# Performance work log

Hardware: AMD Instinct MI355X
Metric: run time of the kernel (lower is better)

Reference implementation:

```python
import jax, jax.numpy as jnp
import numpy as np

N, T, ENC_H, ATT_H, DEC_H, OUT, SPK = 32, 4096, 512, 256, 512, 80, 64
ATT_RANGE = 10
KW = 31  # conv kernel width, padding 15


def softsign(x):
    return x / (1.0 + jnp.abs(x))


def setup_inputs() -> dict:
    key = jax.random.key(0)
    ks = jax.random.split(key, 20)
    lengths_enc = jax.random.randint(ks[0], (N,), 2048, T + 1)
    pos = jnp.arange(T)
    prev_attention = jax.random.uniform(ks[1], (N, T, 1), jnp.float32)
    # zero attention beyond valid length (so argmax lies within length, as in practice)
    prev_attention = prev_attention * (pos[None, :, None] < lengths_enc[:, None, None])
    s = 0.05
    inp = {
        "input_enc": jax.random.normal(ks[2], (N, T, ENC_H), jnp.float32),
        "input_dec": jax.random.normal(ks[3], (N, 1, OUT), jnp.float32),
        "prev_attention": prev_attention,
        "spkr_vec": jax.random.normal(ks[4], (N, 1, SPK), jnp.float32),
        "lengths_enc": lengths_enc,
        "speed": jax.random.uniform(ks[5], (N,), jnp.float32),
        # parameters (torch Linear: y = x @ W.T + b; we store W already transposed)
        "W_enc": jax.random.normal(ks[6], (ENC_H, ATT_H), jnp.float32) * s,
        "b_enc": jnp.zeros((ATT_H,), jnp.float32),
        "W_spkr": jax.random.normal(ks[7], (SPK, ATT_H), jnp.float32) * s,
        "conv_w": jax.random.normal(ks[8], (ATT_H, 1, KW), jnp.float32) * s,  # OIH
        "W_dec": jax.random.normal(ks[9], (DEC_H, ATT_H), jnp.float32) * s,
        "W_speed": jax.random.normal(ks[10], (1, ATT_H), jnp.float32) * s,
        "Wp1": jax.random.normal(ks[11], (OUT + SPK, 2 * DEC_H), jnp.float32) * s,
        "bp1": jnp.zeros((2 * DEC_H,), jnp.float32),
        "Wp2": jax.random.normal(ks[12], (2 * DEC_H, DEC_H), jnp.float32) * s,
        "bp2": jnp.zeros((DEC_H,), jnp.float32),
        "W_proj": jax.random.normal(ks[13], (ATT_H, 1), jnp.float32) * s,
        "b_proj": jnp.zeros((1,), jnp.float32),
    }
    return inp


def reference(input_enc, input_dec, prev_attention, spkr_vec, lengths_enc, speed,
              W_enc, b_enc, W_spkr, conv_w, W_dec, W_speed,
              Wp1, bp1, Wp2, bp2, W_proj, b_proj):
    # prenet (dropout = identity in eval mode)
    dec_in = jnp.concatenate([input_dec, spkr_vec], axis=-1)          # [N,1,OUT+SPK]
    h = jax.nn.relu(dec_in @ Wp1 + bp1)                               # [N,1,2*DEC_H]
    out_prenet = jax.nn.relu(h @ Wp2 + bp2)                           # [N,1,DEC_H]

    # biases (computed fresh, null_bias branch)
    att_bias_speed = (speed[:, None] @ W_speed)[:, None, :]           # [N,1,ATT_H]
    att_bias_enc = softsign(input_enc @ W_enc + b_enc)                # [N,T,ATT_H]
    att_bias_spkr = softsign(spkr_vec @ W_spkr)                       # [N,1,ATT_H]

    # location conv: [N,T,1] -> [N,1,T] -> conv(k=31,p=15) -> [N,ATT_H,T] -> [N,T,ATT_H]
    conv = jax.lax.conv_general_dilated(
        prev_attention.transpose(0, 2, 1), conv_w,
        window_strides=(1,), padding=[(15, 15)],
        dimension_numbers=("NCH", "OIH", "NCH"))
    in_att_prev_att = conv.transpose(0, 2, 1)                         # [N,T,ATT_H]

    in_att_dec = out_prenet @ W_dec                                   # [N,1,ATT_H]

    e = att_bias_enc + in_att_dec + att_bias_spkr + in_att_prev_att + att_bias_speed
    logit = jnp.tanh(e) @ W_proj + b_proj                             # [N,T,1]

    # windowed band mask around argmax of prev attention (no_grad in torch)
    max_idx = jnp.argmax(prev_attention[:, :, 0], axis=1)             # [N]
    lo = jnp.maximum(max_idx - (ATT_RANGE - 1), 0)
    hi = jnp.minimum(max_idx + (ATT_RANGE - 1), lengths_enc - 1)
    pos = jnp.arange(T)
    att_mask = ((pos[None, :] >= lo[:, None]) & (pos[None, :] <= hi[:, None]))
    att_mask = att_mask[:, :, None].astype(logit.dtype)               # [N,T,1]

    logit_max = jnp.max(logit, axis=1, keepdims=True)
    curr = jnp.exp(logit - logit_max) * att_mask
    denom = jnp.maximum(jnp.sum(jnp.abs(curr), axis=1, keepdims=True), 1e-12)
    return curr / denom
```

## Files before the change

kernel.cpp:

```cpp
#include <hip/hip_runtime.h>
#include <hip/hip_bf16.h>

#define NB     32
#define TLEN   4096
#define ENCH   512
#define ATTH   256
#define OUTD   80
#define SPKD   64
#define KW     31
#define ATTR   10

__global__ __launch_bounds__(1024) void prep_kernel(
    const float* __restrict__ pa,
    const float* __restrict__ input_dec,
    const float* __restrict__ spkr_vec,
    const float* __restrict__ speed,
    const float* __restrict__ Wp1,
    const float* __restrict__ bp1,
    const float* __restrict__ Wp2,
    const float* __restrict__ bp2,
    const float* __restrict__ W_dec,
    const float* __restrict__ W_spkr,
    const float* __restrict__ W_speed,
    const int*   __restrict__ lengths,
    float* __restrict__ out,
    int* __restrict__ ws_idx,
    float* __restrict__ ws_bias)
{
  const int n   = blockIdx.x;
  const int tid = threadIdx.x;

  __shared__ float s_dec[144];
  __shared__ float s_h1[1024];
  __shared__ float s_op[512];
  __shared__ __align__(16) float s_red[8 * 512];
  __shared__ float s_av[1024];
  __shared__ int   s_ai[1024];

  ((float4*)(out + (size_t)n * TLEN))[tid] = make_float4(0.f, 0.f, 0.f, 0.f);

  if (tid < OUTD)      s_dec[tid] = input_dec[n * OUTD + tid];
  else if (tid < 144)  s_dec[tid] = spkr_vec[n * SPKD + (tid - OUTD)];

  {
    const float* p = pa + (size_t)n * TLEN;
    float bv = -1.f; int bi = 0;
    #pragma unroll
    for (int k = 0; k < TLEN / 1024; k++) {
      int t = tid + k * 1024;
      float v = p[t];
      if (v > bv) { bv = v; bi = t; }
    }
    s_av[tid] = bv; s_ai[tid] = bi;
    __syncthreads();
    for (int s = 512; s > 0; s >>= 1) {
      if (tid < s) {
        float ov = s_av[tid + s]; int oi = s_ai[tid + s];
        float mv = s_av[tid];     int mi = s_ai[tid];
        if (ov > mv || (ov == mv && oi < mi)) { s_av[tid] = ov; s_ai[tid] = oi; }
      }
      __syncthreads();
    }
    if (tid == 0) {
      int mi = s_ai[0];
      ws_idx[n * 2]     = max(mi - (ATTR - 1), 0);
      ws_idx[n * 2 + 1] = min(mi + (ATTR - 1), lengths[n] - 1);
    }
  }

  {
    float acc = bp1[tid];
    #pragma unroll 4
    for (int i = 0; i < 144; i++)
      acc = fmaf(s_dec[i], Wp1[i * 1024 + tid], acc);
    s_h1[tid] = fmaxf(acc, 0.f);
  }
  __syncthreads();

  {
    const int g = tid & 127, sl = tid >> 7;
    const int k0 = g * 4;
    float4 acc = make_float4(0.f, 0.f, 0.f, 0.f);
    for (int j = sl; j < 1024; j += 8) {
      float hv = s_h1[j];
      float4 w = *(const float4*)(Wp2 + (size_t)j * 512 + k0);
      acc.x = fmaf(hv, w.x, acc.x);
      acc.y = fmaf(hv, w.y, acc.y);
      acc.z = fmaf(hv, w.z, acc.z);
      acc.w = fmaf(hv, w.w, acc.w);
    }
    *(float4*)(s_red + sl * 512 + k0) = acc;
    __syncthreads();
    if (tid < 512) {
      float v = bp2[tid];
      #pragma unroll
      for (int s2 = 0; s2 < 8; s2++) v += s_red[s2 * 512 + tid];
      s_op[tid] = fmaxf(v, 0.f);
    }
    __syncthreads();
  }

  {
    const int c = tid & 255, sl = tid >> 8;
    float acc = 0.f;
    const int kb = sl * 128;
    #pragma unroll 4
    for (int k = kb; k < kb + 128; k++)
      acc = fmaf(s_op[k], W_dec[k * 256 + c], acc);
    s_red[sl * 256 + c] = acc;
    __syncthreads();
    if (tid < 256) {
      float b = s_red[tid] + s_red[256 + tid] + s_red[512 + tid] + s_red[768 + tid];
      float sp = 0.f;
      #pragma unroll 4
      for (int i = 0; i < 64; i++)
        sp = fmaf(s_dec[OUTD + i], W_spkr[i * 256 + tid], sp);
      sp = sp / (1.f + fabsf(sp));
      ws_bias[n * 256 + tid] = b + sp + speed[n] * W_speed[tid];
    }
  }
}

__global__ __launch_bounds__(256) void band_kernel(
    const float* __restrict__ input_enc,
    const float* __restrict__ pa,
    const float* __restrict__ W_enc,
    const float* __restrict__ b_enc,
    const float* __restrict__ conv_w,
    const float* __restrict__ W_proj,
    const int*   __restrict__ ws_idx,
    const float* __restrict__ ws_bias,
    float* __restrict__ ws_logits)
{
  const int n   = blockIdx.x;
  const int j   = blockIdx.y;
  const int tid = threadIdx.x;

  const int lo = ws_idx[n * 2];
  const int hi = ws_idx[n * 2 + 1];
  const int t  = lo + j;

  if (t > hi) {
    if (tid == 0) ws_logits[n * 20 + j] = -__builtin_inff();
    return;
  }

  __shared__ __align__(16) float s_enc[ENCH];
  __shared__ float s_pa[KW];
  __shared__ __align__(16) float s_red[4 * 256];
  __shared__ float s_cw[ATTH * KW];
  __shared__ float s_part[4];

  for (int k2 = tid; k2 < ATTH * KW; k2 += 256) s_cw[k2] = conv_w[k2];
  if (tid < 128)
    ((float4*)s_enc)[tid] = ((const float4*)(input_enc + ((size_t)n * TLEN + t) * ENCH))[tid];
  else if (tid < 128 + KW) {
    int idx = t - (KW / 2) + (tid - 128);
    s_pa[tid - 128] = (idx >= 0 && idx < TLEN) ? pa[(size_t)n * TLEN + idx] : 0.f;
  }
  __syncthreads();

  {
    const int sl = tid >> 6;
    const int l4 = tid & 63;
    const float4* W4 = (const float4*)W_enc;
    float4 acc = make_float4(0.f, 0.f, 0.f, 0.f);
    const int i0 = sl * 128;
    #pragma unroll 8
    for (int i = i0; i < i0 + 128; i++) {
      float e  = s_enc[i];
      float4 w = W4[i * 64 + l4];
      acc.x = fmaf(e, w.x, acc.x);
      acc.y = fmaf(e, w.y, acc.y);
      acc.z = fmaf(e, w.z, acc.z);
      acc.w = fmaf(e, w.w, acc.w);
    }
    *(float4*)(s_red + sl * 256 + l4 * 4) = acc;
  }
  __syncthreads();

  {
    const int c = tid;
    float y = s_red[c] + s_red[256 + c] + s_red[512 + c] + s_red[768 + c];
    float cv = 0.f;
    #pragma unroll
    for (int k = 0; k < KW; k++)
      cv = fmaf(s_pa[k], s_cw[c * KW + k], cv);
    float ss = y + b_enc[c];
    ss = ss / (1.f + fabsf(ss));
    float v = tanhf(ss + ws_bias[n * 256 + c] + cv) * W_proj[c];

    #pragma unroll
    for (int off = 32; off > 0; off >>= 1) v += __shfl_down(v, off);
    if ((tid & 63) == 0) s_part[tid >> 6] = v;
  }
  __syncthreads();
  if (tid == 0)
    ws_logits[n * 20 + j] = s_part[0] + s_part[1] + s_part[2] + s_part[3];
}

__global__ __launch_bounds__(64) void softmax_kernel(
    const float* __restrict__ ws_logits,
    const int*   __restrict__ ws_idx,
    float* __restrict__ out)
{
  const int n   = blockIdx.x;
  const int tid = threadIdx.x;
  const int lo  = ws_idx[n * 2];
  const int hi  = ws_idx[n * 2 + 1];

  float l = (tid < 20) ? ws_logits[n * 20 + tid] : -__builtin_inff();
  float m = l;
  #pragma unroll
  for (int off = 32; off > 0; off >>= 1) m = fmaxf(m, __shfl_down(m, off));
  m = __shfl(m, 0);
  float e = __expf(l - m);
  float s = e;
  #pragma unroll
  for (int off = 32; off > 0; off >>= 1) s += __shfl_down(s, off);
  s = __shfl(s, 0);

  int t = lo + tid;
  if (tid < 20 && t <= hi)
    out[(size_t)n * TLEN + t] = e / s;
}

extern "C" void kernel_launch(void* const* d_in, const int* in_sizes, int n_in,
                              void* d_out, int out_size, void* d_ws, size_t ws_size,
                              hipStream_t stream) {
  const float* input_enc = (const float*)d_in[0];
  const float* input_dec = (const float*)d_in[1];
  const float* pa        = (const float*)d_in[2];
  const float* spkr_vec  = (const float*)d_in[3];
  const int*   lengths   = (const int*)  d_in[4];
  const float* speed     = (const float*)d_in[5];
  const float* W_enc     = (const float*)d_in[6];
  const float* b_enc     = (const float*)d_in[7];
  const float* W_spkr    = (const float*)d_in[8];
  const float* conv_w    = (const float*)d_in[9];
  const float* W_dec     = (const float*)d_in[10];
  const float* W_speed   = (const float*)d_in[11];
  const float* Wp1       = (const float*)d_in[12];
  const float* bp1       = (const float*)d_in[13];
  const float* Wp2       = (const float*)d_in[14];
  const float* bp2       = (const float*)d_in[15];
  const float* W_proj    = (const float*)d_in[16];

  float* out = (float*)d_out;

  int*   ws_idx    = (int*)d_ws;
  float* ws_bias   = (float*)((char*)d_ws + 256);
  float* ws_logits = (float*)((char*)d_ws + 256 + NB * 256 * 4);

  hipLaunchKernelGGL(prep_kernel, dim3(NB), dim3(1024), 0, stream,
                     pa, input_dec, spkr_vec, speed, Wp1, bp1, Wp2, bp2,
                     W_dec, W_spkr, W_speed, lengths, out, ws_idx, ws_bias);

  hipLaunchKernelGGL(band_kernel, dim3(NB, 20), dim3(256), 0, stream,
                     input_enc, pa, W_enc, b_enc, conv_w, W_proj,
                     ws_idx, ws_bias, ws_logits);

  hipLaunchKernelGGL(softmax_kernel, dim3(NB), dim3(64), 0, stream,
                     ws_logits, ws_idx, out);
}
```

Measured before the change: 441.1 us.

## Fuse pipeline into single cooperative kernel with grid syncs and batched prenet

Replaces the three-kernel pipeline with one cooperative kernel of 640 blocks that splits the prenet matmuls across many blocks, batching all 32 samples per weight column, and separates the stages with grid.sync. The softmax is folded in using an atomic counter so the last band block per sample normalises the logits. The goal is to remove the serial 32-block prep kernel, which reads whole weight matrices per sample, and to cut the extra launch overheads. The cost is three grid-wide barriers, a dependence on cooperative launch being supported (with a fallback to the old path), and the band stage no longer staging conv weights in shared memory.

```diff
diff --git a/kernel.cpp b/kernel.cpp
--- a/kernel.cpp
+++ b/kernel.cpp
@@ -1,5 +1,8 @@
 #include <hip/hip_runtime.h>
 #include <hip/hip_bf16.h>
+#include <hip/hip_cooperative_groups.h>
+
+namespace cg = cooperative_groups;
 
 #define NB     32
 #define TLEN   4096
@@ -10,26 +13,238 @@
 #define KW     31
 #define ATTR   10
 
+__global__ __launch_bounds__(256, 4) void coop_kernel(
+    const float* __restrict__ input_enc, const float* __restrict__ input_dec,
+    const float* __restrict__ pa,        const float* __restrict__ spkr_vec,
+    const int*   __restrict__ lengths,   const float* __restrict__ speed,
+    const float* __restrict__ W_enc,     const float* __restrict__ b_enc,
+    const float* __restrict__ W_spkr,    const float* __restrict__ conv_w,
+    const float* __restrict__ W_dec,     const float* __restrict__ W_speed,
+    const float* __restrict__ Wp1,       const float* __restrict__ bp1,
+    const float* __restrict__ Wp2,       const float* __restrict__ bp2,
+    const float* __restrict__ W_proj,    float* __restrict__ out,
+    int* __restrict__ ws_lohi,           int* __restrict__ ws_cnt,
+    float* __restrict__ ws_h1,           float* __restrict__ ws_op,
+    float* __restrict__ ws_bias,         float* __restrict__ ws_logits)
+{
+  const int b   = blockIdx.x;
+  const int tid = threadIdx.x;
+  __shared__ __align__(16) float smem[8192];
+  cg::grid_group grid = cg::this_grid();
+
+  if (b < 64) {
+    const int c0 = b * 16;
+    float* s_dec = smem;
+    float* s_w1  = smem + 4640;
+    for (int idx = tid; idx < 4608; idx += 256) {
+      int m = idx / 144, r = idx - m * 144;
+      s_dec[m * 145 + r] = (r < OUTD) ? input_dec[m * OUTD + r]
+                                      : spkr_vec[m * SPKD + (r - OUTD)];
+    }
+    for (int idx = tid; idx < 2304; idx += 256) {
+      int i = idx >> 4, c = idx & 15;
+      s_w1[idx] = Wp1[i * 1024 + c0 + c];
+    }
+    __syncthreads();
+    const int m = tid & 31, q = tid >> 5;
+    float a0 = 0.f, a1 = 0.f;
+    #pragma unroll 8
+    for (int i = 0; i < 144; i++) {
+      float d = s_dec[m * 145 + i];
+      a0 = fmaf(d, s_w1[i * 16 + q],     a0);
+      a1 = fmaf(d, s_w1[i * 16 + q + 8], a1);
+    }
+    ws_h1[(c0 + q)     * 32 + m] = fmaxf(a0 + bp1[c0 + q],     0.f);
+    ws_h1[(c0 + q + 8) * 32 + m] = fmaxf(a1 + bp1[c0 + q + 8], 0.f);
+  } else if (b < 96) {
+    const int n = b - 64;
+    float* s_v = smem;
+    int*   s_i = (int*)(smem + 256);
+    const float* p = pa + (size_t)n * TLEN;
+    float bv = -1.f; int bi = 0;
+    #pragma unroll
+    for (int k = 0; k < 16; k++) {
+      int t = tid + k * 256;
+      float v = p[t];
+      if (v > bv) { bv = v; bi = t; }
+    }
+    s_v[tid] = bv; s_i[tid] = bi;
+    __syncthreads();
+    for (int s = 128; s > 0; s >>= 1) {
+      if (tid < s) {
+        float ov = s_v[tid + s]; int oi = s_i[tid + s];
+        if (ov > s_v[tid] || (ov == s_v[tid] && oi < s_i[tid])) {
+          s_v[tid] = ov; s_i[tid] = oi;
+        }
+      }
+      __syncthreads();
+    }
+    if (tid == 0) {
+      int mi = s_i[0];
+      ws_lohi[n * 2]     = max(mi - (ATTR - 1), 0);
+      ws_lohi[n * 2 + 1] = min(mi + (ATTR - 1), lengths[n] - 1);
+    }
+  } else if (b < 224) {
+    ((float4*)out)[(b - 96) * 256 + tid] = make_float4(0.f, 0.f, 0.f, 0.f);
+  } else if (b == 224) {
+    if (tid < NB) ws_cnt[tid] = 0;
+  }
+  grid.sync();
+
+  if (b < 128) {
+    const int c0 = b * 4;
+    float* s_w2 = smem;
+    float* s_hh = smem + 4096;
+    for (int idx = tid; idx < 4096; idx += 256) {
+      int r = idx >> 2, c = idx & 3;
+      s_w2[idx] = Wp2[r * 512 + c0 + c];
+    }
+    const int m = tid & 31, q = tid >> 5, c = q & 3, ks = q >> 2;
+    float acc = 0.f;
+    for (int kb = 0; kb < 8; kb++) {
+      if (kb) __syncthreads();
+      for (int idx = tid; idx < 4096; idx += 256)
+        s_hh[idx] = ws_h1[kb * 4096 + idx];
+      __syncthreads();
+      const int ib = ks * 64;
+      #pragma unroll 8
+      for (int i2 = 0; i2 < 64; i2++) {
+        int i = ib + i2;
+        acc = fmaf(s_hh[i * 32 + m], s_w2[(kb * 128 + i) * 4 + c], acc);
+      }
+    }
+    __syncthreads();
+    smem[tid] = acc;
+    __syncthreads();
+    if (ks == 0) {
+      float tot = smem[tid] + smem[tid + 128];
+      ws_op[(c0 + c) * 32 + m] = fmaxf(tot + bp2[c0 + c], 0.f);
+    }
+  }
+  grid.sync();
+
+  if (b < 128) {
+    const int c0 = b * 2;
+    float* s_wd  = smem;
+    float* s_red = smem + 2048;
+    for (int idx = tid; idx < 1024; idx += 256) {
+      int r = idx >> 1, cc = idx & 1;
+      s_wd[idx] = W_dec[r * 256 + c0 + cc];
+    }
+    __syncthreads();
+    const int m = tid & 31, q = tid >> 5, c = q & 1, ks = q >> 1;
+    float acc = 0.f;
+    const int kb = ks * 128;
+    #pragma unroll 8
+    for (int i2 = 0; i2 < 128; i2++) {
+      int k = kb + i2;
+      acc = fmaf(ws_op[k * 32 + m], s_wd[k * 2 + c], acc);
+    }
+    s_red[tid] = acc;
+    __syncthreads();
+    if (q < 2) {
+      float tot = s_red[(0 * 2 + c) * 32 + m] + s_red[(1 * 2 + c) * 32 + m]
+                + s_red[(2 * 2 + c) * 32 + m] + s_red[(3 * 2 + c) * 32 + m];
+      float sp = 0.f;
+      #pragma unroll 8
+      for (int i = 0; i < SPKD; i++)
+        sp = fmaf(spkr_vec[m * SPKD + i], W_spkr[i * 256 + c0 + c], sp);
+      sp = sp / (1.f + fabsf(sp));
+      ws_bias[m * 256 + c0 + c] = tot + sp + speed[m] * W_speed[c0 + c];
+    }
+  }
+  grid.sync();
+
+  {
+    const int n = b / 20;
+    const int j = b - n * 20;
+    const int lo = ws_lohi[n * 2], hi = ws_lohi[n * 2 + 1];
+    const int t  = lo + j;
+    const bool valid = (t <= hi);
+
+    float* s_enc  = smem;
+    float* s_red  = smem + 512;
+    float* s_pa   = smem + 1536;
+    float* s_part = smem + 1568;
+    int*   s_old  = (int*)(smem + 1572);
+
+    if (valid) {
+      if (tid < 128)
+        ((float4*)s_enc)[tid] =
+            ((const float4*)(input_enc + ((size_t)n * TLEN + t) * ENCH))[tid];
+      else if (tid < 128 + KW) {
+        int idx = t - (KW / 2) + (tid - 128);
+        s_pa[tid - 128] = (idx >= 0 && idx < TLEN) ? pa[(size_t)n * TLEN + idx] : 0.f;
+      }
+      __syncthreads();
+      const int sl = tid >> 6, l4 = tid & 63;
+      const float4* W4 = (const float4*)W_enc;
+      float4 a4 = make_float4(0.f, 0.f, 0.f, 0.f);
+      const int i0 = sl * 128;
+      #pragma unroll 8
+      for (int i = i0; i < i0 + 128; i++) {
+        float e  = s_enc[i];
+        float4 w = W4[i * 64 + l4];
+        a4.x = fmaf(e, w.x, a4.x);
+        a4.y = fmaf(e, w.y, a4.y);
+        a4.z = fmaf(e, w.z, a4.z);
+        a4.w = fmaf(e, w.w, a4.w);
+      }
+      *(float4*)(s_red + sl * 256 + l4 * 4) = a4;
+      __syncthreads();
+      const int c = tid;
+      float y = s_red[c] + s_red[256 + c] + s_red[512 + c] + s_red[768 + c];
+      float cv = 0.f;
+      #pragma unroll
+      for (int k = 0; k < KW; k++)
+        cv = fmaf(s_pa[k], conv_w[c * KW + k], cv);
+      float ss = y + b_enc[c];
+      ss = ss / (1.f + fabsf(ss));
+      float v = tanhf(ss + ws_bias[n * 256 + c] + cv) * W_proj[c];
+      #pragma unroll
+      for (int off = 32; off > 0; off >>= 1) v += __shfl_down(v, off);
+      if ((tid & 63) == 0) s_part[tid >> 6] = v;
+      __syncthreads();
+      if (tid == 0)
+        ws_logits[n * 20 + j] = s_part[0] + s_part[1] + s_part[2] + s_part[3];
+    } else {
+      if (tid == 0) ws_logits[n * 20 + j] = -__builtin_inff();
+    }
+
+    if (tid == 0) {
+      __threadfence();
+      *s_old = atomicAdd(&ws_cnt[n], 1);
+    }
+    __syncthreads();
+    if (*s_old == 19 && tid < 64) {
+      __threadfence();
+      float l = (tid < 20) ? ws_logits[n * 20 + tid] : -__builtin_inff();
+      float m2 = l;
+      #pragma unroll
+      for (int off = 32; off > 0; off >>= 1) m2 = fmaxf(m2, __shfl_down(m2, off));
+      m2 = __shfl(m2, 0);
+      float e = __expf(l - m2);
+      float s = e;
+      #pragma unroll
+      for (int off = 32; off > 0; off >>= 1) s += __shfl_down(s, off);
+      s = __shfl(s, 0);
+      int tt = lo + tid;
+      if (tid < 20 && tt <= hi)
+        out[(size_t)n * TLEN + tt] = e / s;
+    }
+  }
+}
+
 __global__ __launch_bounds__(1024) void prep_kernel(
-    const float* __restrict__ pa,
-    const float* __restrict__ input_dec,
-    const float* __restrict__ spkr_vec,
-    const float* __restrict__ speed,
-    const float* __restrict__ Wp1,
-    const float* __restrict__ bp1,
-    const float* __restrict__ Wp2,
-    const float* __restrict__ bp2,
-    const float* __restrict__ W_dec,
-    const float* __restrict__ W_spkr,
-    const float* __restrict__ W_speed,
-    const int*   __restrict__ lengths,
-    float* __restrict__ out,
-    int* __restrict__ ws_idx,
-    float* __restrict__ ws_bias)
+    const float* __restrict__ pa, const float* __restrict__ input_dec,
+    const float* __restrict__ spkr_vec, const float* __restrict__ speed,
+    const float* __restrict__ Wp1, const float* __restrict__ bp1,
+    const float* __restrict__ Wp2, const float* __restrict__ bp2,
+    const float* __restrict__ W_dec, const float* __restrict__ W_spkr,
+    const float* __restrict__ W_speed, const int* __restrict__ lengths,
+    float* __restrict__ out, int* __restrict__ ws_idx, float* __restrict__ ws_bias)
 {
-  const int n   = blockIdx.x;
-  const int tid = threadIdx.x;
-
+  const int n = blockIdx.x, tid = threadIdx.x;
   __shared__ float s_dec[144];
   __shared__ float s_h1[1024];
   __shared__ float s_op[512];
@@ -38,10 +253,8 @@
   __shared__ int   s_ai[1024];
 
   ((float4*)(out + (size_t)n * TLEN))[tid] = make_float4(0.f, 0.f, 0.f, 0.f);
-
   if (tid < OUTD)      s_dec[tid] = input_dec[n * OUTD + tid];
   else if (tid < 144)  s_dec[tid] = spkr_vec[n * SPKD + (tid - OUTD)];
-
   {
     const float* p = pa + (size_t)n * TLEN;
     float bv = -1.f; int bi = 0;
@@ -67,16 +280,13 @@
       ws_idx[n * 2 + 1] = min(mi + (ATTR - 1), lengths[n] - 1);
     }
   }
-
   {
     float acc = bp1[tid];
     #pragma unroll 4
-    for (int i = 0; i < 144; i++)
-      acc = fmaf(s_dec[i], Wp1[i * 1024 + tid], acc);
+    for (int i = 0; i < 144; i++) acc = fmaf(s_dec[i], Wp1[i * 1024 + tid], acc);
     s_h1[tid] = fmaxf(acc, 0.f);
   }
   __syncthreads();
-
   {
     const int g = tid & 127, sl = tid >> 7;
     const int k0 = g * 4;
@@ -84,10 +294,8 @@
     for (int j = sl; j < 1024; j += 8) {
       float hv = s_h1[j];
       float4 w = *(const float4*)(Wp2 + (size_t)j * 512 + k0);
-      acc.x = fmaf(hv, w.x, acc.x);
-      acc.y = fmaf(hv, w.y, acc.y);
-      acc.z = fmaf(hv, w.z, acc.z);
-      acc.w = fmaf(hv, w.w, acc.w);
+      acc.x = fmaf(hv, w.x, acc.x); acc.y = fmaf(hv, w.y, acc.y);
+      acc.z = fmaf(hv, w.z, acc.z); acc.w = fmaf(hv, w.w, acc.w);
     }
     *(float4*)(s_red + sl * 512 + k0) = acc;
     __syncthreads();
@@ -99,51 +307,36 @@
     }
     __syncthreads();
   }
-
   {
     const int c = tid & 255, sl = tid >> 8;
     float acc = 0.f;
     const int kb = sl * 128;
     #pragma unroll 4
-    for (int k = kb; k < kb + 128; k++)
-      acc = fmaf(s_op[k], W_dec[k * 256 + c], acc);
+    for (int k = kb; k < kb + 128; k++) acc = fmaf(s_op[k], W_dec[k * 256 + c], acc);
     s_red[sl * 256 + c] = acc;
     __syncthreads();
     if (tid < 256) {
-      float b = s_red[tid] + s_red[256 + tid] + s_red[512 + tid] + s_red[768 + tid];
+      float b2 = s_red[tid] + s_red[256 + tid] + s_red[512 + tid] + s_red[768 + tid];
       float sp = 0.f;
       #pragma unroll 4
-      for (int i = 0; i < 64; i++)
-        sp = fmaf(s_dec[OUTD + i], W_spkr[i * 256 + tid], sp);
+      for (int i = 0; i < 64; i++) sp = fmaf(s_dec[OUTD + i], W_spkr[i * 256 + tid], sp);
       sp = sp / (1.f + fabsf(sp));
-      ws_bias[n * 256 + tid] = b + sp + speed[n] * W_speed[tid];
+      ws_bias[n * 256 + tid] = b2 + sp + speed[n] * W_speed[tid];
     }
   }
 }
 
 __global__ __launch_bounds__(256) void band_kernel(
-    const float* __restrict__ input_enc,
-    const float* __restrict__ pa,
-    const float* __restrict__ W_enc,
-    const float* __restrict__ b_enc,
-    const float* __restrict__ conv_w,
-    const float* __restrict__ W_proj,
-    const int*   __restrict__ ws_idx,
-    const float* __restrict__ ws_bias,
+    const float* __restrict__ input_enc, const float* __restrict__ pa,
+    const float* __restrict__ W_enc, const float* __restrict__ b_enc,
+    const float* __restrict__ conv_w, const float* __restrict__ W_proj,
+    const int* __restrict__ ws_idx, const float* __restrict__ ws_bias,
     float* __restrict__ ws_logits)
 {
-  const int n   = blockIdx.x;
-  const int j   = blockIdx.y;
-  const int tid = threadIdx.x;
-
-  const int lo = ws_idx[n * 2];
-  const int hi = ws_idx[n * 2 + 1];
-  const int t  = lo + j;
-
-  if (t > hi) {
-    if (tid == 0) ws_logits[n * 20 + j] = -__builtin_inff();
-    return;
-  }
+  const int n = blockIdx.x, j = blockIdx.y, tid = threadIdx.x;
+  const int lo = ws_idx[n * 2], hi = ws_idx[n * 2 + 1];
+  const int t = lo + j;
+  if (t > hi) { if (tid == 0) ws_logits[n * 20 + j] = -__builtin_inff(); return; }
 
   __shared__ __align__(16) float s_enc[ENCH];
   __shared__ float s_pa[KW];
@@ -159,37 +352,30 @@
     s_pa[tid - 128] = (idx >= 0 && idx < TLEN) ? pa[(size_t)n * TLEN + idx] : 0.f;
   }
   __syncthreads();
-
-  {
-    const int sl = tid >> 6;
-    const int l4 = tid & 63;
+  {
+    const int sl = tid >> 6, l4 = tid & 63;
     const float4* W4 = (const float4*)W_enc;
     float4 acc = make_float4(0.f, 0.f, 0.f, 0.f);
     const int i0 = sl * 128;
     #pragma unroll 8
     for (int i = i0; i < i0 + 128; i++) {
-      float e  = s_enc[i];
+      float e = s_enc[i];
       float4 w = W4[i * 64 + l4];
-      acc.x = fmaf(e, w.x, acc.x);
-      acc.y = fmaf(e, w.y, acc.y);
-      acc.z = fmaf(e, w.z, acc.z);
-      acc.w = fmaf(e, w.w, acc.w);
+      acc.x = fmaf(e, w.x, acc.x); acc.y = fmaf(e, w.y, acc.y);
+      acc.z = fmaf(e, w.z, acc.z); acc.w = fmaf(e, w.w, acc.w);
     }
     *(float4*)(s_red + sl * 256 + l4 * 4) = acc;
   }
   __syncthreads();
-
   {
     const int c = tid;
     float y = s_red[c] + s_red[256 + c] + s_red[512 + c] + s_red[768 + c];
     float cv = 0.f;
     #pragma unroll
-    for (int k = 0; k < KW; k++)
-      cv = fmaf(s_pa[k], s_cw[c * KW + k], cv);
+    for (int k = 0; k < KW; k++) cv = fmaf(s_pa[k], s_cw[c * KW + k], cv);
     float ss = y + b_enc[c];
     ss = ss / (1.f + fabsf(ss));
     float v = tanhf(ss + ws_bias[n * 256 + c] + cv) * W_proj[c];
-
     #pragma unroll
     for (int off = 32; off > 0; off >>= 1) v += __shfl_down(v, off);
     if ((tid & 63) == 0) s_part[tid >> 6] = v;
@@ -200,15 +386,11 @@
 }
 
 __global__ __launch_bounds__(64) void softmax_kernel(
-    const float* __restrict__ ws_logits,
-    const int*   __restrict__ ws_idx,
+    const float* __restrict__ ws_logits, const int* __restrict__ ws_idx,
     float* __restrict__ out)
 {
-  const int n   = blockIdx.x;
-  const int tid = threadIdx.x;
-  const int lo  = ws_idx[n * 2];
-  const int hi  = ws_idx[n * 2 + 1];
-
+  const int n = blockIdx.x, tid = threadIdx.x;
+  const int lo = ws_idx[n * 2], hi = ws_idx[n * 2 + 1];
   float l = (tid < 20) ? ws_logits[n * 20 + tid] : -__builtin_inff();
   float m = l;
   #pragma unroll
@@ -219,10 +401,8 @@
   #pragma unroll
   for (int off = 32; off > 0; off >>= 1) s += __shfl_down(s, off);
   s = __shfl(s, 0);
-
   int t = lo + tid;
-  if (tid < 20 && t <= hi)
-    out[(size_t)n * TLEN + t] = e / s;
+  if (tid < 20 && t <= hi) out[(size_t)n * TLEN + t] = e / s;
 }
 
 extern "C" void kernel_launch(void* const* d_in, const int* in_sizes, int n_in,
@@ -248,18 +428,35 @@
 
   float* out = (float*)d_out;
 
-  int*   ws_idx    = (int*)d_ws;
-  float* ws_bias   = (float*)((char*)d_ws + 256);
-  float* ws_logits = (float*)((char*)d_ws + 256 + NB * 256 * 4);
-
-  hipLaunchKernelGGL(prep_kernel, dim3(NB), dim3(1024), 0, stream,
-                     pa, input_dec, spkr_vec, speed, Wp1, bp1, Wp2, bp2,
-                     W_dec, W_spkr, W_speed, lengths, out, ws_idx, ws_bias);
-
-  hipLaunchKernelGGL(band_kernel, dim3(NB, 20), dim3(256), 0, stream,
-                     input_enc, pa, W_enc, b_enc, conv_w, W_proj,
-                     ws_idx, ws_bias, ws_logits);
-
-  hipLaunchKernelGGL(softmax_kernel, dim3(NB), dim3(64), 0, stream,
-                     ws_logits, ws_idx, out);
+  int*   ws_lohi   = (int*)d_ws;
+  int*   ws_cnt    = (int*)((char*)d_ws + 256);
+  float* ws_h1     = (float*)((char*)d_ws + 1024);
+  float* ws_op     = (float*)((char*)d_ws + 1024 + 131072);
+  float* ws_bias   = (float*)((char*)d_ws + 1024 + 131072 + 65536);
+  float* ws_logits = (float*)((char*)d_ws + 1024 + 131072 + 65536 + 32768);
+
+  void* args[] = {
+    (void*)&input_enc, (void*)&input_dec, (void*)&pa, (void*)&spkr_vec,
+    (void*)&lengths, (void*)&speed, (void*)&W_enc, (void*)&b_enc,
+    (void*)&W_spkr, (void*)&conv_w, (void*)&W_dec, (void*)&W_speed,
+    (void*)&Wp1, (void*)&bp1, (void*)&Wp2, (void*)&bp2, (void*)&W_proj,
+    (void*)&out, (void*)&ws_lohi, (void*)&ws_cnt, (void*)&ws_h1,
+    (void*)&ws_op, (void*)&ws_bias, (void*)&ws_logits
+  };
+  hipError_t err = hipLaunchCooperativeKernel((const void*)coop_kernel,
+                                              dim3(NB * 20), dim3(256),
+                                              args, 0, stream);
+  if (err != hipSuccess) {
+    int*   f_idx    = (int*)d_ws;
+    float* f_bias   = (float*)((char*)d_ws + 256);
+    float* f_logits = (float*)((char*)d_ws + 256 + NB * 256 * 4);
+    hipLaunchKernelGGL(prep_kernel, dim3(NB), dim3(1024), 0, stream,
+                       pa, input_dec, spkr_vec, speed, Wp1, bp1, Wp2, bp2,
+                       W_dec, W_spkr, W_speed, lengths, out, f_idx, f_bias);
+    hipLaunchKernelGGL(band_kernel, dim3(NB, 20), dim3(256), 0, stream,
+                       input_enc, pa, W_enc, b_enc, conv_w, W_proj,
+                       f_idx, f_bias, f_logits);
+    hipLaunchKernelGGL(softmax_kernel, dim3(NB), dim3(64), 0, stream,
+                       f_logits, f_idx, out);
+  }
 }
```

New measurement: 629.1 us. 1.43x slower.
